# Kernel tuning notes

Measured on AMD Instinct MI355X. Metric: run time of the kernel, lower is better.

## Reference

```python
import jax, jax.numpy as jnp
from jax import lax
import numpy as np

B, H, W, C = 512, 64, 128, 3
FEAT = 13 * 26 * 64  # ceil(64/5)*ceil(128/5)*(32+32) after SAME stride-5 convs + concat


def setup_inputs() -> dict:
    key = jax.random.key(0)
    ks = jax.random.split(key, 6)
    x = jax.random.normal(ks[0], (B, H, W, C), jnp.float32)
    conv0_w = jax.random.normal(ks[1], (3, 3, 3, 32), jnp.float32) * 0.05  # HWIO
    conv1_w = jax.random.normal(ks[2], (5, 5, 3, 32), jnp.float32) * 0.05
    fc0_w = jax.random.normal(ks[3], (FEAT, 32), jnp.float32) * 0.01
    fc0_b = jnp.zeros((32,), jnp.float32)
    fc1_w = jax.random.normal(ks[4], (32, 6), jnp.float32) * 0.1
    fc1_b = jnp.zeros((6,), jnp.float32)
    return {"x": x, "conv0_w": conv0_w, "conv1_w": conv1_w,
            "fc0_w": fc0_w, "fc0_b": fc0_b, "fc1_w": fc1_w, "fc1_b": fc1_b}


def _stn_forward(x, conv0_w, conv1_w, fc0_w, fc0_b, fc1_w, fc1_b):
    b, h, w, c = x.shape
    dn = ("NHWC", "HWIO", "NHWC")
    # ---- LocNet ----
    # AveragePooling2D(3x3, stride 1, SAME); TF avg_pool averages over valid
    # (non-padded) elements only, so normalize by a window-count map.
    psum = lax.reduce_window(x, 0.0, lax.add, (1, 3, 3, 1), (1, 1, 1, 1), "SAME")
    cnt = lax.reduce_window(jnp.ones((1, h, w, 1), x.dtype), 0.0, lax.add,
                            (1, 3, 3, 1), (1, 1, 1, 1), "SAME")
    pooled = psum / cnt
    x0 = jax.nn.relu(lax.conv_general_dilated(pooled, conv0_w, (5, 5), "SAME",
                                              dimension_numbers=dn))
    x1 = jax.nn.relu(lax.conv_general_dilated(x, conv1_w, (5, 5), "SAME",
                                              dimension_numbers=dn))
    feat = jnp.concatenate([x0, x1], axis=-1).reshape(b, -1)
    # Dropout(0.5) is identity at inference.
    hid = jnp.tanh(feat @ fc0_w + fc0_b)
    theta = jnp.tanh(hid @ fc1_w + fc1_b).reshape(b, 2, 3)
    # ---- gen_grid ----
    xt, yt = jnp.meshgrid(jnp.linspace(-1.0, 1.0, w), jnp.linspace(-1.0, 1.0, h))
    grid = jnp.stack([xt.ravel(), yt.ravel(), jnp.ones(h * w, x.dtype)])  # [3, h*w]
    T = jnp.einsum("bij,jk->bik", theta, grid)          # [b, 2, h*w]
    T = T.reshape(b, 2, h, w).transpose(0, 2, 3, 1)     # [b, h, w, 2]
    # ---- grid_sample (bilinear) ----
    gx = (T[..., 0] + 1.0) * w / 2.0
    gy = (T[..., 1] + 1.0) * h / 2.0
    x0f = jnp.clip(jnp.floor(gx), 0.0, w - 2.0)
    x1f = jnp.clip(jnp.floor(gx) + 1.0, 1.0, w - 1.0)
    y0f = jnp.clip(jnp.floor(gy), 0.0, h - 2.0)
    y1f = jnp.clip(jnp.floor(gy) + 1.0, 1.0, h - 1.0)
    xi0, xi1 = x0f.astype(jnp.int32), x1f.astype(jnp.int32)
    yi0, yi1 = y0f.astype(jnp.int32), y1f.astype(jnp.int32)
    bi = jnp.arange(b)[:, None, None]                   # broadcast batch index
    Q00 = x[bi, yi0, xi0]  # [b, h, w, c]
    Q01 = x[bi, yi1, xi0]
    Q10 = x[bi, yi0, xi1]
    Q11 = x[bi, yi1, xi1]
    wx0 = (x1f - gx)[..., None]
    wx1 = (gx - x0f)[..., None]
    wy0 = (y1f - gy)[..., None]
    wy1 = (gy - y0f)[..., None]
    # Wx @ Q @ Wy expanded: rows of Q are x-neighbors, cols are y-neighbors.
    out = wx0 * (wy0 * Q00 + wy1 * Q01) + wx1 * (wy0 * Q10 + wy1 * Q11)
    Wd = ((x1f - x0f) * (y1f - y0f))[..., None]
    return out / Wd


def reference(x, conv0_w, conv1_w, fc0_w, fc0_b, fc1_w, fc1_b):
    return _stn_forward(x, conv0_w, conv1_w, fc0_w, fc0_b, fc1_w, fc1_b)
```

## Files before the change

### kernel.cpp

```cpp
#include <hip/hip_runtime.h>
#include <math.h>

namespace {
constexpr int BN = 512, HH = 64, WW = 128, CC = 3;
constexpr int OHH = 13, OWW = 26;
constexpr int NPOS = OHH * OWW;
constexpr int PCH = 26;
constexpr int NPC = NPOS / PCH;
}

__global__ __launch_bounds__(256, 3) void k_locnet(const float* __restrict__ x,
                                                   const float* __restrict__ w0,
                                                   const float* __restrict__ w1,
                                                   const float* __restrict__ fw0,
                                                   float* __restrict__ part) {
  __shared__ float lds[6400];
  const int L = (blockIdx.x & 7) * (NPOS * 8 / 8) + (blockIdx.x >> 3);
  const int bc = L / NPOS;
  const int pos = L - bc * NPOS;
  const int oh = pos / OWW, ow = pos - oh * OWW;
  const int b0 = bc * 64;

  for (int k = 0; k < 24; ++k) {
    const int f = threadIdx.x + (k << 8);
    const int bi = f / 96;
    const int r = f - bi * 96;
    const int ri = r >> 4, s = r & 15;
    if (s < 15) {
      const int j = s / 3, ic = s - j * 3;
      const int gr = oh * 5 - 1 + ri;
      const int gc = ow * 5 - 1 + j;
      float v = 0.f;
      if (gr >= 0 && gr < HH && gc >= 0 && gc < WW)
        v = x[(size_t)(b0 + bi) * (HH * WW * CC) + gr * (WW * CC) + gc * CC + ic];
      lds[bi * 91 + ri * 15 + s] = v;
    }
  }
  __syncthreads();

  const int wv = __builtin_amdgcn_readfirstlane(threadIdx.x >> 6);
  const int bl = threadIdx.x & 63;
  float xr[90];
  {
    const int xbase = bl * 91;
#pragma unroll
    for (int t2 = 0; t2 < 90; ++t2) xr[t2] = lds[xbase + t2];
  }

  float hacc[32];
#pragma unroll
  for (int n = 0; n < 32; ++n) hacc[n] = 0.f;

  float pooled[27];
#pragma unroll
  for (int kh = 0; kh < 3; ++kh)
#pragma unroll
    for (int kw = 0; kw < 3; ++kw) {
      const int gr = oh * 5 + kh, gc = ow * 5 + kw;
      const int rc = min(gr + 1, HH - 1) - max(gr - 1, 0) + 1;
      const int c2 = min(gc + 1, WW - 1) - max(gc - 1, 0) + 1;
      const float inv = 1.0f / (float)(rc * c2);
#pragma unroll
      for (int ic = 0; ic < 3; ++ic) {
        float s = 0.f;
#pragma unroll
        for (int dr = 0; dr < 3; ++dr)
#pragma unroll
          for (int dc = 0; dc < 3; ++dc)
            s += xr[(kh + dr) * 15 + (kw + dc) * 3 + ic];
        pooled[(kh * 3 + kw) * 3 + ic] = s * inv;
      }
    }

  {
    float a[8] = {0.f, 0.f, 0.f, 0.f, 0.f, 0.f, 0.f, 0.f};
#pragma unroll
    for (int tap = 0; tap < 27; ++tap) {
      const float pv = pooled[tap];
      const float4 wa = *(const float4*)(w0 + tap * 32 + wv * 8);
      const float4 wb = *(const float4*)(w0 + tap * 32 + wv * 8 + 4);
      a[0] += pv * wa.x; a[1] += pv * wa.y; a[2] += pv * wa.z; a[3] += pv * wa.w;
      a[4] += pv * wb.x; a[5] += pv * wb.y; a[6] += pv * wb.z; a[7] += pv * wb.w;
    }
#pragma unroll
    for (int j = 0; j < 8; ++j) {
      const float aj = fmaxf(a[j], 0.f);
      const float* wr = fw0 + (size_t)(pos * 64 + wv * 8 + j) * 32;
#pragma unroll
      for (int q = 0; q < 8; ++q) {
        const float4 w4 = *(const float4*)(wr + q * 4);
        hacc[q * 4 + 0] += aj * w4.x; hacc[q * 4 + 1] += aj * w4.y;
        hacc[q * 4 + 2] += aj * w4.z; hacc[q * 4 + 3] += aj * w4.w;
      }
    }
  }

  {
    float a[8] = {0.f, 0.f, 0.f, 0.f, 0.f, 0.f, 0.f, 0.f};
#pragma unroll
    for (int kh = 0; kh < 5; ++kh)
#pragma unroll
      for (int kw = 0; kw < 5; ++kw)
#pragma unroll
        for (int ic = 0; ic < 3; ++ic) {
          const float pv = xr[(kh + 1) * 15 + kw * 3 + ic];
          const int tap = (kh * 5 + kw) * 3 + ic;
          const float4 wa = *(const float4*)(w1 + tap * 32 + wv * 8);
          const float4 wb = *(const float4*)(w1 + tap * 32 + wv * 8 + 4);
          a[0] += pv * wa.x; a[1] += pv * wa.y; a[2] += pv * wa.z; a[3] += pv * wa.w;
          a[4] += pv * wb.x; a[5] += pv * wb.y; a[6] += pv * wb.z; a[7] += pv * wb.w;
        }
#pragma unroll
    for (int j = 0; j < 8; ++j) {
      const float aj = fmaxf(a[j], 0.f);
      const float* wr = fw0 + (size_t)(pos * 64 + 32 + wv * 8 + j) * 32;
#pragma unroll
      for (int q = 0; q < 8; ++q) {
        const float4 w4 = *(const float4*)(wr + q * 4);
        hacc[q * 4 + 0] += aj * w4.x; hacc[q * 4 + 1] += aj * w4.y;
        hacc[q * 4 + 2] += aj * w4.z; hacc[q * 4 + 3] += aj * w4.w;
      }
    }
  }

  __syncthreads();
  if (wv > 0) {
    float* rp = &lds[(size_t)(wv - 1) * 64 * 33 + bl * 33];
#pragma unroll
    for (int n = 0; n < 32; ++n) rp[n] = hacc[n];
  }
  __syncthreads();
  if (wv == 0) {
    float* po = part + (size_t)pos * 32 * 512 + b0 + bl;
#pragma unroll
    for (int n = 0; n < 32; ++n) {
      const float s = hacc[n] + lds[bl * 33 + n] + lds[64 * 33 + bl * 33 + n] +
                      lds[128 * 33 + bl * 33 + n];
      po[(size_t)n * 512] = s;
    }
  }
}

__global__ __launch_bounds__(256) void k_theta1(const float* __restrict__ part,
                                                float* __restrict__ part2) {
  const int pc = blockIdx.x >> 3;
  const int bcs = blockIdx.x & 7;
  const int lane = threadIdx.x & 63;
  const int og = threadIdx.x >> 6;
  const int bcol = bcs * 64 + lane;
  float acc[8] = {0.f, 0.f, 0.f, 0.f, 0.f, 0.f, 0.f, 0.f};
  const float* pp = part + ((size_t)pc * PCH * 32 + og * 8) * 512 + bcol;
  for (int pq = 0; pq < PCH; ++pq) {
#pragma unroll
    for (int j = 0; j < 8; ++j)
      acc[j] += pp[((size_t)pq * 32 + j) * 512];
  }
  float* o = part2 + ((size_t)pc * 32 + og * 8) * 512 + bcol;
#pragma unroll
  for (int j = 0; j < 8; ++j) o[(size_t)j * 512] = acc[j];
}

__global__ __launch_bounds__(256) void k_theta2(const float* __restrict__ part2,
                                                const float* __restrict__ b0,
                                                const float* __restrict__ w1f,
                                                const float* __restrict__ b1,
                                                float* __restrict__ theta) {
  __shared__ float hid[64][32];
  const int lane = threadIdx.x & 63;
  const int og = threadIdx.x >> 6;
  const int bcol = blockIdx.x * 64 + lane;
#pragma unroll
  for (int j = 0; j < 8; ++j) {
    const int oc = og * 8 + j;
    float s = b0[oc];
#pragma unroll
    for (int pc = 0; pc < NPC; ++pc)
      s += part2[((size_t)pc * 32 + oc) * 512 + bcol];
    hid[lane][oc] = tanhf(s);
  }
  __syncthreads();
  for (int u = threadIdx.x; u < 64 * 6; u += 256) {
    const int bl = u / 6, j = u - bl * 6;
    float s2 = b1[j];
#pragma unroll
    for (int oc = 0; oc < 32; ++oc) s2 += hid[bl][oc] * w1f[oc * 6 + j];
    theta[(blockIdx.x * 64 + bl) * 6 + j] = tanhf(s2);
  }
}

__global__ __launch_bounds__(256) void k_sample(const float* __restrict__ x,
                                                const float* __restrict__ theta,
                                                float* __restrict__ out) {
  const int b = blockIdx.x >> 3;
  const int seg = blockIdx.x & 7;
  __shared__ float th[6];
  if (threadIdx.x < 6) th[threadIdx.x] = theta[b * 6 + threadIdx.x];
  __syncthreads();
  const float t00 = th[0], t01 = th[1], t02 = th[2];
  const float t10 = th[3], t11 = th[4], t12 = th[5];
  const int idx = seg * 1024 + threadIdx.x * 4;
  const int i = idx >> 7, j0 = idx & 127;
  const float yt = (float)i * (2.0f / 63.0f) - 1.0f;
  const float* xb = x + (size_t)b * (HH * WW * CC);
  float res[12];
#pragma unroll
  for (int p = 0; p < 4; ++p) {
    const float xt = (float)(j0 + p) * (2.0f / 127.0f) - 1.0f;
    const float gx = (t00 * xt + t01 * yt + t02 + 1.0f) * 64.0f;
    const float gy = (t10 * xt + t11 * yt + t12 + 1.0f) * 32.0f;
    const float fx = floorf(gx), fy = floorf(gy);
    const float x0f = fminf(fmaxf(fx, 0.f), 126.f);
    const float x1f = fminf(fmaxf(fx + 1.f, 1.f), 127.f);
    const float y0f = fminf(fmaxf(fy, 0.f), 62.f);
    const float y1f = fminf(fmaxf(fy + 1.f, 1.f), 63.f);
    const float wx0 = x1f - gx, wx1 = gx - x0f;
    const float wy0 = y1f - gy, wy1 = gy - y0f;
    const int xi0 = (int)x0f, xi1 = (int)x1f;
    const int yi0 = (int)y0f, yi1 = (int)y1f;
    const float* q00 = xb + (yi0 * WW + xi0) * 3;
    const float* q01 = xb + (yi1 * WW + xi0) * 3;
    const float* q10 = xb + (yi0 * WW + xi1) * 3;
    const float* q11 = xb + (yi1 * WW + xi1) * 3;
#pragma unroll
    for (int c = 0; c < 3; ++c)
      res[p * 3 + c] = wx0 * (wy0 * q00[c] + wy1 * q01[c]) +
                       wx1 * (wy0 * q10[c] + wy1 * q11[c]);
  }
  float4* o = (float4*)(out + ((size_t)b * 8192 + idx) * 3);
  o[0] = make_float4(res[0], res[1], res[2], res[3]);
  o[1] = make_float4(res[4], res[5], res[6], res[7]);
  o[2] = make_float4(res[8], res[9], res[10], res[11]);
}

extern "C" void kernel_launch(void* const* d_in, const int* in_sizes, int n_in,
                              void* d_out, int out_size, void* d_ws, size_t ws_size,
                              hipStream_t stream) {
  (void)in_sizes; (void)n_in; (void)out_size; (void)ws_size;
  const float* x   = (const float*)d_in[0];
  const float* w0  = (const float*)d_in[1];
  const float* w1  = (const float*)d_in[2];
  const float* fw0 = (const float*)d_in[3];
  const float* fb0 = (const float*)d_in[4];
  const float* fw1 = (const float*)d_in[5];
  const float* fb1 = (const float*)d_in[6];
  float* outp = (float*)d_out;
  float* part  = outp;
  float* part2 = outp + (size_t)NPOS * 32 * 512;
  float* theta = (float*)d_ws;
  k_locnet<<<NPOS * 8, 256, 0, stream>>>(x, w0, w1, fw0, part);
  k_theta1<<<NPC * 8, 256, 0, stream>>>(part, part2);
  k_theta2<<<8, 256, 0, stream>>>(part2, fb0, fw1, fb1, theta);
  k_sample<<<BN * 8, 256, 0, stream>>>(x, theta, outp);
}
```

Measured before the change: 151.3 us.

## Compute avg-pool cooperatively into LDS and drop per-thread register patch

The 3x3 average pooling is now computed once per (tap, batch) pair by all threads and stored in a second LDS region, instead of each of the four waves redundantly pooling in registers. The 90-float per-thread register copy of the input patch is removed, and conv taps are read directly from LDS. This is meant to cut register pressure and redundant pooling work, at the cost of an extra barrier and more LDS traffic in the conv loops. The launch-bounds occupancy hint is dropped and the raw-patch load loop is compacted from 96-wide to 90-wide rows.

```diff
diff --git a/kernel.cpp b/kernel.cpp
--- a/kernel.cpp
+++ b/kernel.cpp
@@ -7,76 +7,72 @@
 constexpr int NPOS = OHH * OWW;
 constexpr int PCH = 26;
 constexpr int NPC = NPOS / PCH;
-}
-
-__global__ __launch_bounds__(256, 3) void k_locnet(const float* __restrict__ x,
-                                                   const float* __restrict__ w0,
-                                                   const float* __restrict__ w1,
-                                                   const float* __restrict__ fw0,
-                                                   float* __restrict__ part) {
-  __shared__ float lds[6400];
-  const int L = (blockIdx.x & 7) * (NPOS * 8 / 8) + (blockIdx.x >> 3);
+constexpr int RAWN = 64 * 91;
+constexpr int PLDS0 = RAWN;
+}
+
+__global__ __launch_bounds__(256) void k_locnet(const float* __restrict__ x,
+                                                const float* __restrict__ w0,
+                                                const float* __restrict__ w1,
+                                                const float* __restrict__ fw0,
+                                                float* __restrict__ part) {
+  __shared__ float lds[RAWN + 64 * 29];
+  const int L = (blockIdx.x & 7) * NPOS + (blockIdx.x >> 3);
   const int bc = L / NPOS;
   const int pos = L - bc * NPOS;
   const int oh = pos / OWW, ow = pos - oh * OWW;
   const int b0 = bc * 64;
 
-  for (int k = 0; k < 24; ++k) {
+  for (int k = 0; k < 23; ++k) {
     const int f = threadIdx.x + (k << 8);
-    const int bi = f / 96;
-    const int r = f - bi * 96;
-    const int ri = r >> 4, s = r & 15;
-    if (s < 15) {
-      const int j = s / 3, ic = s - j * 3;
+    if (f < 64 * 90) {
+      const int bi = f / 90;
+      const int pix = f - bi * 90;
+      const int ri = pix / 15;
+      const int rem = pix - ri * 15;
+      const int j = rem / 3, ic = rem - j * 3;
       const int gr = oh * 5 - 1 + ri;
       const int gc = ow * 5 - 1 + j;
       float v = 0.f;
       if (gr >= 0 && gr < HH && gc >= 0 && gc < WW)
-        v = x[(size_t)(b0 + bi) * (HH * WW * CC) + gr * (WW * CC) + gc * CC + ic];
-      lds[bi * 91 + ri * 15 + s] = v;
-    }
-  }
-  __syncthreads();
-
-  const int wv = __builtin_amdgcn_readfirstlane(threadIdx.x >> 6);
-  const int bl = threadIdx.x & 63;
-  float xr[90];
-  {
-    const int xbase = bl * 91;
-#pragma unroll
-    for (int t2 = 0; t2 < 90; ++t2) xr[t2] = lds[xbase + t2];
-  }
-
-  float hacc[32];
-#pragma unroll
-  for (int n = 0; n < 32; ++n) hacc[n] = 0.f;
-
-  float pooled[27];
-#pragma unroll
-  for (int kh = 0; kh < 3; ++kh)
-#pragma unroll
-    for (int kw = 0; kw < 3; ++kw) {
+        v = x[((size_t)(b0 + bi) * HH + gr) * (WW * CC) + gc * CC + ic];
+      lds[bi * 91 + pix] = v;
+    }
+  }
+  __syncthreads();
+
+  for (int k = 0; k < 7; ++k) {
+    const int u = threadIdx.x + (k << 8);
+    if (u < 27 * 64) {
+      const int tap = u >> 6, bi = u & 63;
+      const int khkw = tap / 3, ic = tap - khkw * 3;
+      const int kh = khkw / 3, kw = khkw - kh * 3;
+      float s = 0.f;
+#pragma unroll
+      for (int dr = 0; dr < 3; ++dr)
+#pragma unroll
+        for (int dc = 0; dc < 3; ++dc)
+          s += lds[bi * 91 + (kh + dr) * 15 + (kw + dc) * 3 + ic];
       const int gr = oh * 5 + kh, gc = ow * 5 + kw;
       const int rc = min(gr + 1, HH - 1) - max(gr - 1, 0) + 1;
       const int c2 = min(gc + 1, WW - 1) - max(gc - 1, 0) + 1;
-      const float inv = 1.0f / (float)(rc * c2);
-#pragma unroll
-      for (int ic = 0; ic < 3; ++ic) {
-        float s = 0.f;
-#pragma unroll
-        for (int dr = 0; dr < 3; ++dr)
-#pragma unroll
-          for (int dc = 0; dc < 3; ++dc)
-            s += xr[(kh + dr) * 15 + (kw + dc) * 3 + ic];
-        pooled[(kh * 3 + kw) * 3 + ic] = s * inv;
-      }
-    }
+      lds[PLDS0 + bi * 29 + tap] = s / (float)(rc * c2);
+    }
+  }
+  __syncthreads();
+
+  const int wv = __builtin_amdgcn_readfirstlane(threadIdx.x >> 6);
+  const int bl = threadIdx.x & 63;
+
+  float hacc[32];
+#pragma unroll
+  for (int n = 0; n < 32; ++n) hacc[n] = 0.f;
 
   {
     float a[8] = {0.f, 0.f, 0.f, 0.f, 0.f, 0.f, 0.f, 0.f};
 #pragma unroll
     for (int tap = 0; tap < 27; ++tap) {
-      const float pv = pooled[tap];
+      const float pv = lds[PLDS0 + bl * 29 + tap];
       const float4 wa = *(const float4*)(w0 + tap * 32 + wv * 8);
       const float4 wb = *(const float4*)(w0 + tap * 32 + wv * 8 + 4);
       a[0] += pv * wa.x; a[1] += pv * wa.y; a[2] += pv * wa.z; a[3] += pv * wa.w;
@@ -103,7 +99,7 @@
       for (int kw = 0; kw < 5; ++kw)
 #pragma unroll
         for (int ic = 0; ic < 3; ++ic) {
-          const float pv = xr[(kh + 1) * 15 + kw * 3 + ic];
+          const float pv = lds[bl * 91 + (kh + 1) * 15 + kw * 3 + ic];
           const int tap = (kh * 5 + kw) * 3 + ic;
           const float4 wa = *(const float4*)(w1 + tap * 32 + wv * 8);
           const float4 wb = *(const float4*)(w1 + tap * 32 + wv * 8 + 4);
```

Measured after the change: 151.7 us. No clear change (+0.3%).
